# Performance work log

Hardware: AMD Instinct MI355X
Metric: run time of the kernel (lower is better)

The kernel has to match this reference:

```python
import jax, jax.numpy as jnp
import numpy as np

B, C, H, W = 16, 384, 56, 56
NH, WS, SS = 12, 7, 3          # num_heads, window_size, shift_size
MLP = 4 * C
N = WS * WS                     # tokens per window (49)
nHW = H // WS                   # windows per side (8)
nW = nHW * nHW                  # windows per image (64)
HD = C // NH                    # head dim (32)
EPS = 1e-5


def _ln(x, g, b):
    mu = jnp.mean(x, axis=-1, keepdims=True)
    var = jnp.mean(jnp.square(x - mu), axis=-1, keepdims=True)
    return (x - mu) * jax.lax.rsqrt(var + EPS) * g + b


def _attn_mask():
    # static shifted-window mask, computed once with numpy (constants)
    img = np.zeros((H, W))
    sl = (slice(0, -WS), slice(-WS, -SS), slice(-SS, None))
    cnt = 0
    for hs in sl:
        for ws_ in sl:
            img[hs, ws_] = cnt
            cnt += 1
    mw = img.reshape(nHW, WS, nHW, WS).transpose(0, 2, 1, 3).reshape(-1, N)
    d = mw[:, None, :] - mw[:, :, None]          # (nW, N, N)
    return jnp.asarray(np.where(d != 0, -100.0, 0.0), jnp.float32)

_MASK = _attn_mask()


def setup_inputs() -> dict:
    key = jax.random.key(0)
    ks = jax.random.split(key, 6)
    rn = lambda k, s: jax.random.normal(k, s, jnp.float32) * 0.02
    return {
        "x": jax.random.normal(ks[0], (B, C, H, W), jnp.float32),
        "norm1_g": jnp.ones((C,), jnp.float32),
        "norm1_b": jnp.zeros((C,), jnp.float32),
        "qkv_w": rn(ks[1], (C, 3 * C)),
        "qkv_b": jnp.zeros((3 * C,), jnp.float32),
        "proj_w": rn(ks[2], (C, C)),
        "proj_b": jnp.zeros((C,), jnp.float32),
        "norm2_g": jnp.ones((C,), jnp.float32),
        "norm2_b": jnp.zeros((C,), jnp.float32),
        "fc1_w": rn(ks[3], (C, MLP)),
        "fc1_b": jnp.zeros((MLP,), jnp.float32),
        "fc2_w": rn(ks[4], (MLP, C)),
        "fc2_b": jnp.zeros((C,), jnp.float32),
    }


def reference(x, norm1_g, norm1_b, qkv_w, qkv_b, proj_w, proj_b,
              norm2_g, norm2_b, fc1_w, fc1_b, fc2_w, fc2_b):
    shortcut = x                                   # (B, C, H, W)
    xh = jnp.transpose(x, (0, 2, 3, 1))            # (B, H, W, C)
    xh = _ln(xh, norm1_g, norm1_b)
    # H, W divisible by WS -> padding is a no-op; shifted window path
    xs = jnp.roll(xh, (-SS, -SS), axis=(1, 2))
    # window partition -> (B*nW, N, C)
    xw = xs.reshape(B, nHW, WS, nHW, WS, C).transpose(0, 1, 3, 2, 4, 5)
    xw = xw.reshape(-1, N, C)
    # attention
    qkv = (xw @ qkv_w + qkv_b).reshape(-1, N, 3, NH, HD).transpose(2, 0, 3, 1, 4)
    q, k, v = qkv[0] * HD ** -0.5, qkv[1], qkv[2]  # (B*nW, NH, N, HD)
    attn = jnp.einsum('whnd,whmd->whnm', q, k)     # (B*nW, NH, N, N)
    attn = attn.reshape(B, nW, NH, N, N) + _MASK[None, :, None]
    attn = jax.nn.softmax(attn, axis=-1).reshape(-1, NH, N, N)
    out = jnp.einsum('whnm,whmd->whnd', attn, v)   # (B*nW, NH, N, HD)
    out = out.transpose(0, 2, 1, 3).reshape(-1, N, C)
    out = out @ proj_w + proj_b
    # window reverse -> (B, H, W, C), un-shift
    xs = out.reshape(B, nHW, nHW, WS, WS, C).transpose(0, 1, 3, 2, 4, 5)
    xs = xs.reshape(B, H, W, C)
    xh = jnp.roll(xs, (SS, SS), axis=(1, 2))
    x2 = shortcut + jnp.transpose(xh, (0, 3, 1, 2))
    # MLP residual (in BHWC)
    xh2 = jnp.transpose(x2, (0, 2, 3, 1))
    h = jax.nn.gelu(_ln(xh2, norm2_g, norm2_b) @ fc1_w + fc1_b,
                    approximate=False) @ fc2_w + fc2_b
    xh2 = xh2 + h
    return jnp.transpose(xh2, (0, 3, 1, 2))
```

## Files before the change

kernel.cpp:

```cpp
#include <hip/hip_runtime.h>
#include <hip/hip_bf16.h>
#include <math.h>
#include <stdint.h>

#define C_ 384
#define TOKENS 50176

typedef __bf16 bf16;
typedef __bf16 bf16x8 __attribute__((ext_vector_type(8)));
typedef float  f32x4  __attribute__((ext_vector_type(4)));

__device__ __forceinline__ float b2f(bf16 x) { return (float)x; }
__device__ __forceinline__ bf16  f2b(float x) { return (bf16)x; }

__device__ __forceinline__ void gld_lds16(const bf16* g, bf16* l) {
    __builtin_amdgcn_global_load_lds(
        (const __attribute__((address_space(1))) void*)g,
        (__attribute__((address_space(3))) void*)l, 16, 0, 0);
}

__global__ void wtrans_kernel(const float* __restrict__ in, bf16* __restrict__ out,
                              int K, int N) {
    int idx = blockIdx.x * 256 + threadIdx.x;
    if (idx >= K * N) return;
    int n = idx / K, k = idx % K;
    out[idx] = f2b(in[(size_t)k * N + n]);
}

__global__ __launch_bounds__(256) void ln1_gather_kernel(
    const float* __restrict__ x, const float* __restrict__ g,
    const float* __restrict__ bt, bf16* __restrict__ xw) {
    int wave = threadIdx.x >> 6, lane = threadIdx.x & 63;
    int T = blockIdx.x * 4 + wave;
    int wi = T / 49, n = T % 49;
    int b = wi >> 6, w64 = wi & 63;
    int bh = w64 >> 3, bw = w64 & 7;
    int hs = bh * 7 + n / 7 + 3; if (hs >= 56) hs -= 56;
    int wsd = bw * 7 + n % 7 + 3; if (wsd >= 56) wsd -= 56;
    const float* xp = x + (size_t)b * C_ * 3136 + hs * 56 + wsd;
    float v[6];
    #pragma unroll
    for (int k = 0; k < 6; k++) v[k] = xp[(size_t)(lane + k * 64) * 3136];
    float s = v[0] + v[1] + v[2] + v[3] + v[4] + v[5];
    #pragma unroll
    for (int m = 32; m; m >>= 1) s += __shfl_xor(s, m);
    float mu = s * (1.0f / 384.0f);
    float s2 = 0.f;
    #pragma unroll
    for (int k = 0; k < 6; k++) { float d = v[k] - mu; s2 += d * d; }
    #pragma unroll
    for (int m = 32; m; m >>= 1) s2 += __shfl_xor(s2, m);
    float rstd = rsqrtf(s2 * (1.0f / 384.0f) + 1e-5f);
    bf16* op = xw + (size_t)T * 384;
    #pragma unroll
    for (int k = 0; k < 6; k++) {
        int c = lane + k * 64;
        op[c] = f2b((v[k] - mu) * rstd * g[c] + bt[c]);
    }
}

enum { EPI_NONE = 0, EPI_GELU = 1, EPI_PROJ = 2, EPI_FC2 = 3 };

template <int EPI>
__global__ __launch_bounds__(256) void gemm_kernel(
    const bf16* __restrict__ A, const bf16* __restrict__ Wt,
    const float* __restrict__ bias, bf16* __restrict__ Cout,
    int Kdim, int Ndim,
    const float* __restrict__ resx,
    const bf16* __restrict__ resb) {
    __shared__ __align__(16) bf16 As[128 * 32];
    __shared__ __align__(16) bf16 Bs[128 * 32];
    int t = threadIdx.x;
    int m0 = blockIdx.x * 128, n0 = blockIdx.y * 128;
    int lane = t & 63, wave = t >> 6;
    int wr = wave >> 1, wc = wave & 1;
    int quad = lane >> 4, lm = lane & 15;
    f32x4 acc[4][4] = {};

    int c1 = t, c2 = t + 256;
    const bf16* ga1 = A + (size_t)(m0 + (c1 >> 2)) * Kdim + (c1 & 3) * 8;
    const bf16* ga2 = A + (size_t)(m0 + (c2 >> 2)) * Kdim + (c2 & 3) * 8;
    const bf16* gb1 = Wt + (size_t)(n0 + (c1 >> 2)) * Kdim + (c1 & 3) * 8;
    const bf16* gb2 = Wt + (size_t)(n0 + (c2 >> 2)) * Kdim + (c2 & 3) * 8;
    bf16* la1 = As + c1 * 8; bf16* la2 = As + c2 * 8;
    bf16* lb1 = Bs + c1 * 8; bf16* lb2 = Bs + c2 * 8;

    for (int k0 = 0; k0 < Kdim; k0 += 32) {
        gld_lds16(ga1 + k0, la1);
        gld_lds16(ga2 + k0, la2);
        gld_lds16(gb1 + k0, lb1);
        gld_lds16(gb2 + k0, lb2);
        __syncthreads();
        bf16x8 af[4], bfr[4];
        #pragma unroll
        for (int i = 0; i < 4; i++)
            af[i] = *(const bf16x8*)(As + (wr * 64 + i * 16 + lm) * 32 + quad * 8);
        #pragma unroll
        for (int j = 0; j < 4; j++)
            bfr[j] = *(const bf16x8*)(Bs + (wc * 64 + j * 16 + lm) * 32 + quad * 8);
        #pragma unroll
        for (int i = 0; i < 4; i++)
            #pragma unroll
            for (int j = 0; j < 4; j++)
                acc[i][j] = __builtin_amdgcn_mfma_f32_16x16x32_bf16(af[i], bfr[j], acc[i][j], 0, 0, 0);
        __syncthreads();
    }

    int col[4]; float bv[4];
    #pragma unroll
    for (int j = 0; j < 4; j++) { col[j] = n0 + wc * 64 + j * 16 + lm; bv[j] = bias[col[j]]; }
    #pragma unroll
    for (int i = 0; i < 4; i++) {
        #pragma unroll
        for (int r = 0; r < 4; r++) {
            int row = m0 + wr * 64 + i * 16 + quad * 4 + r;
            size_t resbase = 0;
            if (EPI == EPI_PROJ) {
                int wi = row / 49, n = row % 49;
                int b = wi >> 6, w64 = wi & 63;
                int bh = w64 >> 3, bw = w64 & 7;
                int hs = bh * 7 + n / 7 + 3; if (hs >= 56) hs -= 56;
                int wsd = bw * 7 + n % 7 + 3; if (wsd >= 56) wsd -= 56;
                resbase = (size_t)b * C_ * 3136 + hs * 56 + wsd;
            }
            #pragma unroll
            for (int j = 0; j < 4; j++) {
                float v = acc[i][j][r] + bv[j];
                if (EPI == EPI_GELU) v = 0.5f * v * (1.0f + erff(v * 0.70710678118f));
                if (EPI == EPI_PROJ) v += resx[resbase + (size_t)col[j] * 3136];
                if (EPI == EPI_FC2)  v += b2f(resb[(size_t)row * 384 + col[j]]);
                Cout[(size_t)row * Ndim + col[j]] = f2b(v);
            }
        }
    }
}

__global__ __launch_bounds__(64) void attn_mfma_kernel(const bf16* __restrict__ qkv,
                                                       bf16* __restrict__ aout) {
    __shared__ __align__(16) bf16 pbuf[64 * 72];
    __shared__ int reg_[64];
    int l = threadIdx.x;
    int wi = blockIdx.x / 12, h = blockIdx.x % 12;
    int i16 = l & 15, quad = l >> 4;

    {
        int tok = l < 49 ? l : 48;
        int w64 = wi & 63;
        int bh = w64 >> 3, bw = w64 & 7;
        int hh = bh * 7 + tok / 7, ww = bw * 7 + tok % 7;
        int fh = hh < 49 ? 0 : (hh < 53 ? 1 : 2);
        int fw = ww < 49 ? 0 : (ww < 53 ? 1 : 2);
        reg_[l] = fh * 3 + fw;
    }
    __syncthreads();

    const bf16* qbase = qkv + (size_t)wi * 49 * 1152 + h * 32;

    f32x4 s_[4][4] = {};
    bf16x8 af[4], bfr[4];
    #pragma unroll
    for (int mi = 0; mi < 4; mi++) {
        int m = mi * 16 + i16; if (m > 48) m = 48;
        af[mi] = *(const bf16x8*)(qbase + (size_t)m * 1152 + quad * 8);
    }
    #pragma unroll
    for (int nt = 0; nt < 4; nt++) {
        int n = nt * 16 + i16; if (n > 48) n = 48;
        bfr[nt] = *(const bf16x8*)(qbase + 384 + (size_t)n * 1152 + quad * 8);
    }
    #pragma unroll
    for (int mi = 0; mi < 4; mi++)
        #pragma unroll
        for (int nt = 0; nt < 4; nt++)
            s_[mi][nt] = __builtin_amdgcn_mfma_f32_16x16x32_bf16(af[mi], bfr[nt], s_[mi][nt], 0, 0, 0);

    int creg[4];
    #pragma unroll
    for (int nt = 0; nt < 4; nt++) {
        int c = nt * 16 + i16; if (c > 48) c = 48;
        creg[nt] = reg_[c];
    }

    const float scale = 0.17677669529663687f;
    #pragma unroll
    for (int mi = 0; mi < 4; mi++) {
        #pragma unroll
        for (int r = 0; r < 4; r++) {
            int row = mi * 16 + quad * 4 + r;
            int rreg = reg_[row];
            float v[4]; float mx = -1e30f;
            #pragma unroll
            for (int nt = 0; nt < 4; nt++) {
                int c = nt * 16 + i16;
                float x = s_[mi][nt][r] * scale;
                if (c > 48) x = -1e30f;
                else if (rreg != creg[nt]) x -= 100.0f;
                v[nt] = x; mx = fmaxf(mx, x);
            }
            #pragma unroll
            for (int m = 8; m; m >>= 1) mx = fmaxf(mx, __shfl_xor(mx, m));
            float sum = 0.f;
            #pragma unroll
            for (int nt = 0; nt < 4; nt++) { v[nt] = __expf(v[nt] - mx); sum += v[nt]; }
            #pragma unroll
            for (int m = 8; m; m >>= 1) sum += __shfl_xor(sum, m);
            float inv = 1.0f / sum;
            #pragma unroll
            for (int nt = 0; nt < 4; nt++)
                pbuf[row * 72 + nt * 16 + i16] = f2b(v[nt] * inv);
        }
    }
    __syncthreads();

    f32x4 o_[4][2] = {};
    const bf16* vbase = qkv + (size_t)wi * 49 * 1152 + 768 + h * 32;
    #pragma unroll
    for (int ks = 0; ks < 2; ks++) {
        bf16x8 pa[4];
        #pragma unroll
        for (int mi = 0; mi < 4; mi++)
            pa[mi] = *(const bf16x8*)(pbuf + (mi * 16 + i16) * 72 + ks * 32 + quad * 8);
        bf16x8 vb[2];
        #pragma unroll
        for (int nt = 0; nt < 2; nt++)
            #pragma unroll
            for (int j = 0; j < 8; j++) {
                int tok = ks * 32 + quad * 8 + j; if (tok > 48) tok = 48;
                vb[nt][j] = vbase[(size_t)tok * 1152 + nt * 16 + i16];
            }
        #pragma unroll
        for (int mi = 0; mi < 4; mi++)
            #pragma unroll
            for (int nt = 0; nt < 2; nt++)
                o_[mi][nt] = __builtin_amdgcn_mfma_f32_16x16x32_bf16(pa[mi], vb[nt], o_[mi][nt], 0, 0, 0);
    }

    bf16* obase = aout + (size_t)wi * 49 * 384 + h * 32;
    #pragma unroll
    for (int mi = 0; mi < 4; mi++)
        #pragma unroll
        for (int r = 0; r < 4; r++) {
            int row = mi * 16 + quad * 4 + r;
            if (row < 49) {
                #pragma unroll
                for (int nt = 0; nt < 2; nt++)
                    obase[(size_t)row * 384 + nt * 16 + i16] = f2b(o_[mi][nt][r]);
            }
        }
}

__global__ __launch_bounds__(256) void ln2_kernel(const bf16* __restrict__ x2,
                                                  const float* __restrict__ g,
                                                  const float* __restrict__ bt,
                                                  bf16* __restrict__ x2n) {
    int wave = threadIdx.x >> 6, lane = threadIdx.x & 63;
    int T = blockIdx.x * 4 + wave;
    const bf16* xp = x2 + (size_t)T * 384;
    float v[6];
    #pragma unroll
    for (int k = 0; k < 6; k++) v[k] = b2f(xp[lane + k * 64]);
    float s = v[0] + v[1] + v[2] + v[3] + v[4] + v[5];
    #pragma unroll
    for (int m = 32; m; m >>= 1) s += __shfl_xor(s, m);
    float mu = s * (1.0f / 384.0f);
    float s2 = 0.f;
    #pragma unroll
    for (int k = 0; k < 6; k++) { float d = v[k] - mu; s2 += d * d; }
    #pragma unroll
    for (int m = 32; m; m >>= 1) s2 += __shfl_xor(s2, m);
    float rstd = rsqrtf(s2 * (1.0f / 384.0f) + 1e-5f);
    bf16* op = x2n + (size_t)T * 384;
    #pragma unroll
    for (int k = 0; k < 6; k++) {
        int c = lane + k * 64;
        op[c] = f2b((v[k] - mu) * rstd * g[c] + bt[c]);
    }
}

__global__ __launch_bounds__(256) void untile_kernel(const bf16* __restrict__ otok,
                                                     float* __restrict__ out) {
    __shared__ float tile[56 * 65];
    int t = threadIdx.x;
    int b = blockIdx.x / 336;
    int rem = blockIdx.x % 336;
    int h = rem / 6;
    int c0 = (rem % 6) * 64;
    int hs = h + 53; if (hs >= 56) hs -= 56;
    int bh = hs / 7, th = hs % 7;
    #pragma unroll
    for (int pass = 0; pass < 14; pass++) {
        int w = pass * 4 + (t >> 6);
        int c = t & 63;
        int wsd = w + 53; if (wsd >= 56) wsd -= 56;
        int T = (b * 64 + bh * 8 + wsd / 7) * 49 + th * 7 + wsd % 7;
        tile[w * 65 + c] = b2f(otok[(size_t)T * 384 + c0 + c]);
    }
    __syncthreads();
    #pragma unroll
    for (int pass = 0; pass < 14; pass++) {
        int idx = pass * 256 + t;
        int c = idx / 56, w = idx % 56;
        out[((size_t)(b * 384 + c0 + c)) * 3136 + h * 56 + w] = tile[w * 65 + c];
    }
}

extern "C" void kernel_launch(void* const* d_in, const int* in_sizes, int n_in,
                              void* d_out, int out_size, void* d_ws, size_t ws_size,
                              hipStream_t stream) {
    (void)in_sizes; (void)n_in; (void)out_size; (void)ws_size;
    const float* x      = (const float*)d_in[0];
    const float* n1g    = (const float*)d_in[1];
    const float* n1b    = (const float*)d_in[2];
    const float* qkv_w  = (const float*)d_in[3];
    const float* qkv_b  = (const float*)d_in[4];
    const float* proj_w = (const float*)d_in[5];
    const float* proj_b = (const float*)d_in[6];
    const float* n2g    = (const float*)d_in[7];
    const float* n2b    = (const float*)d_in[8];
    const float* fc1_w  = (const float*)d_in[9];
    const float* fc1_b  = (const float*)d_in[10];
    const float* fc2_w  = (const float*)d_in[11];
    const float* fc2_b  = (const float*)d_in[12];
    float* out = (float*)d_out;
    char* ws = (char*)d_ws;

    bf16* qkv_wT = (bf16*)(ws + 0);
    bf16* proj_wT = (bf16*)(ws + 884736);
    bf16* fc1_wT = (bf16*)(ws + 1179648);
    bf16* fc2_wT = (bf16*)(ws + 2359296);
    bf16* xw   = (bf16*)(ws + 4194304);
    bf16* qkvb = (bf16*)(ws + 42729472);
    bf16* attn = (bf16*)(ws + 158334976);
    bf16* x2   = (bf16*)(ws + 4194304);
    bf16* x2n  = (bf16*)(ws + 42729472);
    bf16* h1   = (bf16*)(ws + 81264640);
    bf16* otok = (bf16*)(ws + 235405312);

    wtrans_kernel<<<(384 * 1152 + 255) / 256, 256, 0, stream>>>(qkv_w, qkv_wT, 384, 1152);
    wtrans_kernel<<<(384 * 384 + 255) / 256, 256, 0, stream>>>(proj_w, proj_wT, 384, 384);
    wtrans_kernel<<<(384 * 1536 + 255) / 256, 256, 0, stream>>>(fc1_w, fc1_wT, 384, 1536);
    wtrans_kernel<<<(1536 * 384 + 255) / 256, 256, 0, stream>>>(fc2_w, fc2_wT, 1536, 384);

    ln1_gather_kernel<<<TOKENS / 4, 256, 0, stream>>>(x, n1g, n1b, xw);

    gemm_kernel<EPI_NONE><<<dim3(392, 9), 256, 0, stream>>>(
        xw, qkv_wT, qkv_b, qkvb, 384, 1152, nullptr, nullptr);

    attn_mfma_kernel<<<12288, 64, 0, stream>>>(qkvb, attn);

    gemm_kernel<EPI_PROJ><<<dim3(392, 3), 256, 0, stream>>>(
        attn, proj_wT, proj_b, x2, 384, 384, x, nullptr);

    ln2_kernel<<<TOKENS / 4, 256, 0, stream>>>(x2, n2g, n2b, x2n);

    gemm_kernel<EPI_GELU><<<dim3(392, 12), 256, 0, stream>>>(
        x2n, fc1_wT, fc1_b, h1, 384, 1536, nullptr, nullptr);

    gemm_kernel<EPI_FC2><<<dim3(392, 3), 256, 0, stream>>>(
        h1, fc2_wT, fc2_b, otok, 1536, 384, nullptr, x2);

    untile_kernel<<<16 * 336, 256, 0, stream>>>(otok, out);
}
```

Baseline: 738.9 us.

## Widen GEMM K-tile to 64 with XOR-swizzled LDS, transposed MFMA, vectorized epilogue, fast GELU

The GEMM now stages 64-wide K tiles in LDS instead of 32, which halves the number of barrier pairs per K loop. A XOR swizzle on the global source address keeps the LDS reads free of bank conflicts. The MFMA operands are swapped so each lane holds four consecutive output columns, which allows 4-wide bias loads, residual loads and bf16 stores in the epilogue. The erf-based GELU is replaced by a tanh-style sigmoid approximation, which trades a small accuracy loss for fewer instructions. LDS use doubles, which may reduce occupancy.

```diff
diff --git a/kernel.cpp b/kernel.cpp
--- a/kernel.cpp
+++ b/kernel.cpp
@@ -8,10 +8,16 @@
 
 typedef __bf16 bf16;
 typedef __bf16 bf16x8 __attribute__((ext_vector_type(8)));
+typedef __bf16 bf16x4 __attribute__((ext_vector_type(4)));
 typedef float  f32x4  __attribute__((ext_vector_type(4)));
 
 __device__ __forceinline__ float b2f(bf16 x) { return (float)x; }
 __device__ __forceinline__ bf16  f2b(float x) { return (bf16)x; }
+
+__device__ __forceinline__ float fast_gelu(float v) {
+    float u2 = v * fmaf(v * v, 0.07135481f, 1.5957691f);
+    return v / (1.0f + __expf(-u2));
+}
 
 __device__ __forceinline__ void gld_lds16(const bf16* g, bf16* l) {
     __builtin_amdgcn_global_load_lds(
@@ -68,8 +74,8 @@
     int Kdim, int Ndim,
     const float* __restrict__ resx,
     const bf16* __restrict__ resb) {
-    __shared__ __align__(16) bf16 As[128 * 32];
-    __shared__ __align__(16) bf16 Bs[128 * 32];
+    __shared__ __align__(16) bf16 As[128 * 64];
+    __shared__ __align__(16) bf16 Bs[128 * 64];
     int t = threadIdx.x;
     int m0 = blockIdx.x * 128, n0 = blockIdx.y * 128;
     int lane = t & 63, wave = t >> 6;
@@ -77,60 +83,81 @@
     int quad = lane >> 4, lm = lane & 15;
     f32x4 acc[4][4] = {};
 
-    int c1 = t, c2 = t + 256;
-    const bf16* ga1 = A + (size_t)(m0 + (c1 >> 2)) * Kdim + (c1 & 3) * 8;
-    const bf16* ga2 = A + (size_t)(m0 + (c2 >> 2)) * Kdim + (c2 & 3) * 8;
-    const bf16* gb1 = Wt + (size_t)(n0 + (c1 >> 2)) * Kdim + (c1 & 3) * 8;
-    const bf16* gb2 = Wt + (size_t)(n0 + (c2 >> 2)) * Kdim + (c2 & 3) * 8;
-    bf16* la1 = As + c1 * 8; bf16* la2 = As + c2 * 8;
-    bf16* lb1 = Bs + c1 * 8; bf16* lb2 = Bs + c2 * 8;
-
-    for (int k0 = 0; k0 < Kdim; k0 += 32) {
-        gld_lds16(ga1 + k0, la1);
-        gld_lds16(ga2 + k0, la2);
-        gld_lds16(gb1 + k0, lb1);
-        gld_lds16(gb2 + k0, lb2);
+    const bf16* gA[4]; const bf16* gB[4];
+    bf16 *lA[4], *lB[4];
+    #pragma unroll
+    for (int p = 0; p < 4; p++) {
+        int c = p * 256 + t;
+        int row = c >> 3, g = c & 7;
+        int gs = g ^ (row & 7);
+        gA[p] = A  + (size_t)(m0 + row) * Kdim + gs * 8;
+        gB[p] = Wt + (size_t)(n0 + row) * Kdim + gs * 8;
+        lA[p] = As + c * 8;
+        lB[p] = Bs + c * 8;
+    }
+
+    for (int k0 = 0; k0 < Kdim; k0 += 64) {
+        #pragma unroll
+        for (int p = 0; p < 4; p++) {
+            gld_lds16(gA[p] + k0, lA[p]);
+            gld_lds16(gB[p] + k0, lB[p]);
+        }
         __syncthreads();
-        bf16x8 af[4], bfr[4];
-        #pragma unroll
-        for (int i = 0; i < 4; i++)
-            af[i] = *(const bf16x8*)(As + (wr * 64 + i * 16 + lm) * 32 + quad * 8);
-        #pragma unroll
-        for (int j = 0; j < 4; j++)
-            bfr[j] = *(const bf16x8*)(Bs + (wc * 64 + j * 16 + lm) * 32 + quad * 8);
-        #pragma unroll
-        for (int i = 0; i < 4; i++)
+        #pragma unroll
+        for (int kk = 0; kk < 2; kk++) {
+            bf16x8 af[4], bfr[4];
+            int grp = (kk * 4 + quad) ^ (lm & 7);
+            #pragma unroll
+            for (int i = 0; i < 4; i++)
+                af[i] = *(const bf16x8*)(As + (wr * 64 + i * 16 + lm) * 64 + grp * 8);
             #pragma unroll
             for (int j = 0; j < 4; j++)
-                acc[i][j] = __builtin_amdgcn_mfma_f32_16x16x32_bf16(af[i], bfr[j], acc[i][j], 0, 0, 0);
+                bfr[j] = *(const bf16x8*)(Bs + (wc * 64 + j * 16 + lm) * 64 + grp * 8);
+            #pragma unroll
+            for (int j = 0; j < 4; j++)
+                #pragma unroll
+                for (int i = 0; i < 4; i++)
+                    acc[j][i] = __builtin_amdgcn_mfma_f32_16x16x32_bf16(bfr[j], af[i], acc[j][i], 0, 0, 0);
+        }
         __syncthreads();
     }
 
-    int col[4]; float bv[4];
-    #pragma unroll
-    for (int j = 0; j < 4; j++) { col[j] = n0 + wc * 64 + j * 16 + lm; bv[j] = bias[col[j]]; }
     #pragma unroll
     for (int i = 0; i < 4; i++) {
-        #pragma unroll
-        for (int r = 0; r < 4; r++) {
-            int row = m0 + wr * 64 + i * 16 + quad * 4 + r;
-            size_t resbase = 0;
+        int m = m0 + wr * 64 + i * 16 + lm;
+        size_t resbase = 0;
+        if (EPI == EPI_PROJ) {
+            int wi = m / 49, n_ = m % 49;
+            int b = wi >> 6, w64 = wi & 63;
+            int bh = w64 >> 3, bw = w64 & 7;
+            int hs = bh * 7 + n_ / 7 + 3; if (hs >= 56) hs -= 56;
+            int wsd = bw * 7 + n_ % 7 + 3; if (wsd >= 56) wsd -= 56;
+            resbase = (size_t)b * C_ * 3136 + hs * 56 + wsd;
+        }
+        #pragma unroll
+        for (int j = 0; j < 4; j++) {
+            int nb = n0 + wc * 64 + j * 16 + quad * 4;
+            f32x4 bj = *(const f32x4*)(bias + nb);
+            f32x4 v;
+            #pragma unroll
+            for (int r = 0; r < 4; r++) v[r] = acc[j][i][r] + bj[r];
+            if (EPI == EPI_GELU) {
+                #pragma unroll
+                for (int r = 0; r < 4; r++) v[r] = fast_gelu(v[r]);
+            }
             if (EPI == EPI_PROJ) {
-                int wi = row / 49, n = row % 49;
-                int b = wi >> 6, w64 = wi & 63;
-                int bh = w64 >> 3, bw = w64 & 7;
-                int hs = bh * 7 + n / 7 + 3; if (hs >= 56) hs -= 56;
-                int wsd = bw * 7 + n % 7 + 3; if (wsd >= 56) wsd -= 56;
-                resbase = (size_t)b * C_ * 3136 + hs * 56 + wsd;
-            }
-            #pragma unroll
-            for (int j = 0; j < 4; j++) {
-                float v = acc[i][j][r] + bv[j];
-                if (EPI == EPI_GELU) v = 0.5f * v * (1.0f + erff(v * 0.70710678118f));
-                if (EPI == EPI_PROJ) v += resx[resbase + (size_t)col[j] * 3136];
-                if (EPI == EPI_FC2)  v += b2f(resb[(size_t)row * 384 + col[j]]);
-                Cout[(size_t)row * Ndim + col[j]] = f2b(v);
-            }
+                #pragma unroll
+                for (int r = 0; r < 4; r++) v[r] += resx[resbase + (size_t)(nb + r) * 3136];
+            }
+            if (EPI == EPI_FC2) {
+                bf16x4 rb = *(const bf16x4*)(resb + (size_t)m * 384 + nb);
+                #pragma unroll
+                for (int r = 0; r < 4; r++) v[r] += b2f(rb[r]);
+            }
+            bf16x4 o;
+            #pragma unroll
+            for (int r = 0; r < 4; r++) o[r] = f2b(v[r]);
+            *(bf16x4*)(Cout + (size_t)m * Ndim + nb) = o;
         }
     }
 }
```

New measurement: 736.2 us. Within noise of the previous version (-0.4%).
